# Kernel tuning notes

Measured on AMD Instinct MI355X. Metric: run time of the kernel, lower is better.

Reference implementation:

```python
import jax, jax.numpy as jnp
import numpy as np

# Output order of the stacked loss vector (7,):
# [loss_pose_intra_t, loss_pose_inter_t, loss_pose_intra_s, loss_pose_inter_s,
#  loss_pose_t, loss_pose_s, loss_pose]
ALPHA_T = 0.5
ALPHA_S = 0.75
ALPHA_TS = 0.5
EPS = 1e-8


def setup_inputs() -> dict:
    key = jax.random.key(0)
    k1, k2 = jax.random.split(key)
    B, M, C = 32, 784, 4
    pred_dT = jax.random.normal(k1, (B, M, M, C), dtype=jnp.float32)
    gt_dT = jax.random.normal(k2, (B, M, M, C), dtype=jnp.float32)
    # V=4 views, 196 tokens each; sum(Ms) must equal M
    Ms = jnp.full((4,), 196, dtype=jnp.int32)
    return {"pred_dT": pred_dT, "gt_dT": gt_dT, "Ms": Ms}


def reference(pred_dT, gt_dT, Ms):
    B, M, _, C = pred_dT.shape
    V = Ms.shape[0]
    dtype = pred_dT.dtype

    # criterion = 'mse', reduction='none'
    loss_full = (pred_dT - gt_dT) ** 2  # (B, M, M, C)

    # view id per token; same-view (intra) pair mask (M, M)
    view_ids = jnp.repeat(jnp.arange(V), Ms, total_repeat_length=M)
    intra_mask = (view_ids[:, None] == view_ids[None, :]).astype(dtype)

    # per-channel sums over all pairs and over intra-view pairs
    per_ch_all = loss_full.sum(axis=(0, 1, 2))                       # (C,)
    per_ch_intra = jnp.einsum('bijc,ij->c', loss_full, intra_mask)   # (C,)

    total_all_t = per_ch_all[0:2].sum()
    total_all_s = per_ch_all[2:4].sum()
    total_intra_t = per_ch_intra[0:2].sum()
    total_intra_s = per_ch_intra[2:4].sum()
    total_inter_t = total_all_t - total_intra_t
    total_inter_s = total_all_s - total_intra_s

    sum_Ms_sq = jnp.sum(Ms * Ms)
    diag_count = (sum_Ms_sq * B).astype(dtype)
    offdiag_count = ((M * M - sum_Ms_sq) * B).astype(dtype)

    zero = jnp.zeros((), dtype)
    loss_intra_t = jnp.where(diag_count > EPS, total_intra_t / diag_count, zero)
    loss_inter_t = jnp.where(offdiag_count > EPS, total_inter_t / offdiag_count, zero)
    loss_intra_s = jnp.where(diag_count > EPS, total_intra_s / diag_count, zero)
    loss_inter_s = jnp.where(offdiag_count > EPS, total_inter_s / offdiag_count, zero)

    loss_t = ALPHA_T * loss_inter_t + (1.0 - ALPHA_T) * loss_intra_t
    loss_s = ALPHA_S * loss_inter_s + (1.0 - ALPHA_S) * loss_intra_s
    loss = ALPHA_TS * loss_t + (1.0 - ALPHA_TS) * loss_s

    return jnp.stack([loss_intra_t, loss_inter_t, loss_intra_s, loss_inter_s,
                      loss_t, loss_s, loss])
```

## Files before the change

### kernel.cpp

```cpp
#include <hip/hip_runtime.h>

constexpr int B_ = 32;
constexpr int M_ = 784;

constexpr int NBLK = 1792;
constexpr int NTHR = 256;
constexpr int TOTAL  = B_ * M_ * M_;
constexpr int STRIDE = NBLK * NTHR;
constexpr int KFULL  = TOTAL / STRIDE;

constexpr float ALPHA_T  = 0.5f;
constexpr float ALPHA_S  = 0.75f;
constexpr float ALPHA_TS = 0.5f;
constexpr float EPS      = 1e-8f;

__global__ __launch_bounds__(NTHR) void pose_loss_partial_kernel(
    const float4* __restrict__ pred, const float4* __restrict__ gt,
    const int* __restrict__ Ms, float4* __restrict__ partials)
{
    const int cum0 = Ms[0];
    const int cum1 = cum0 + Ms[1];
    const int cum2 = cum1 + Ms[2];

    float all_t = 0.f, all_s = 0.f, intra_t = 0.f, intra_s = 0.f;

    auto body = [&](int idx) {
        const float4 p = pred[idx];
        const float4 g = gt[idx];
        const float d0 = p.x - g.x;
        const float d1 = p.y - g.y;
        const float d2 = p.z - g.z;
        const float d3 = p.w - g.w;
        const float t = d0 * d0 + d1 * d1;
        const float s = d2 * d2 + d3 * d3;
        all_t += t;
        all_s += s;
        const int q = idx / M_;
        const int j = idx - q * M_;
        const int i = q - (q / M_) * M_;
        const int vi = (i >= cum0) + (i >= cum1) + (i >= cum2);
        const int vj = (j >= cum0) + (j >= cum1) + (j >= cum2);
        if (vi == vj) { intra_t += t; intra_s += s; }
    };

    int idx = blockIdx.x * NTHR + threadIdx.x;
    #pragma unroll 2
    for (int k = 0; k < KFULL; ++k, idx += STRIDE) {
        body(idx);
    }
    if (idx < TOTAL) {
        body(idx);
    }

    float v0 = all_t, v1 = all_s, v2 = intra_t, v3 = intra_s;
    #pragma unroll
    for (int off = 32; off > 0; off >>= 1) {
        v0 += __shfl_down(v0, off, 64);
        v1 += __shfl_down(v1, off, 64);
        v2 += __shfl_down(v2, off, 64);
        v3 += __shfl_down(v3, off, 64);
    }

    __shared__ float4 sm[NTHR / 64];
    const int lane = threadIdx.x & 63;
    const int wid  = threadIdx.x >> 6;
    if (lane == 0) sm[wid] = make_float4(v0, v1, v2, v3);
    __syncthreads();

    if (threadIdx.x == 0) {
        float4 acc = sm[0];
        #pragma unroll
        for (int w = 1; w < NTHR / 64; ++w) {
            acc.x += sm[w].x; acc.y += sm[w].y;
            acc.z += sm[w].z; acc.w += sm[w].w;
        }
        partials[blockIdx.x] = acc;
    }
}

__global__ __launch_bounds__(NTHR) void pose_loss_final_kernel(
    const float4* __restrict__ partials, const int* __restrict__ Ms,
    float* __restrict__ out)
{
    float v0 = 0.f, v1 = 0.f, v2 = 0.f, v3 = 0.f;
    for (int p = threadIdx.x; p < NBLK; p += NTHR) {
        const float4 q = partials[p];
        v0 += q.x; v1 += q.y; v2 += q.z; v3 += q.w;
    }
    #pragma unroll
    for (int off = 32; off > 0; off >>= 1) {
        v0 += __shfl_down(v0, off, 64);
        v1 += __shfl_down(v1, off, 64);
        v2 += __shfl_down(v2, off, 64);
        v3 += __shfl_down(v3, off, 64);
    }
    __shared__ float4 sm[NTHR / 64];
    const int lane = threadIdx.x & 63;
    const int wid  = threadIdx.x >> 6;
    if (lane == 0) sm[wid] = make_float4(v0, v1, v2, v3);
    __syncthreads();

    if (threadIdx.x == 0) {
        float4 acc = sm[0];
        #pragma unroll
        for (int w = 1; w < NTHR / 64; ++w) {
            acc.x += sm[w].x; acc.y += sm[w].y;
            acc.z += sm[w].z; acc.w += sm[w].w;
        }
        const float total_all_t   = acc.x;
        const float total_all_s   = acc.y;
        const float total_intra_t = acc.z;
        const float total_intra_s = acc.w;
        const float total_inter_t = total_all_t - total_intra_t;
        const float total_inter_s = total_all_s - total_intra_s;

        int sum_Ms_sq = 0;
        #pragma unroll
        for (int v = 0; v < 4; ++v) sum_Ms_sq += Ms[v] * Ms[v];
        const float diag_count    = (float)((long long)sum_Ms_sq * B_);
        const float offdiag_count = (float)(((long long)M_ * M_ - sum_Ms_sq) * B_);

        const float li_t = (diag_count    > EPS) ? total_intra_t / diag_count    : 0.f;
        const float le_t = (offdiag_count > EPS) ? total_inter_t / offdiag_count : 0.f;
        const float li_s = (diag_count    > EPS) ? total_intra_s / diag_count    : 0.f;
        const float le_s = (offdiag_count > EPS) ? total_inter_s / offdiag_count : 0.f;

        const float loss_t = ALPHA_T  * le_t + (1.f - ALPHA_T)  * li_t;
        const float loss_s = ALPHA_S  * le_s + (1.f - ALPHA_S)  * li_s;
        const float loss   = ALPHA_TS * loss_t + (1.f - ALPHA_TS) * loss_s;

        out[0] = li_t;
        out[1] = le_t;
        out[2] = li_s;
        out[3] = le_s;
        out[4] = loss_t;
        out[5] = loss_s;
        out[6] = loss;
    }
}

extern "C" void kernel_launch(void* const* d_in, const int* in_sizes, int n_in,
                              void* d_out, int out_size, void* d_ws, size_t ws_size,
                              hipStream_t stream) {
    const float4* pred = (const float4*)d_in[0];
    const float4* gt   = (const float4*)d_in[1];
    const int*    Ms   = (const int*)d_in[2];
    float*        out  = (float*)d_out;
    float4*       partials = (float4*)d_ws;

    pose_loss_partial_kernel<<<NBLK, NTHR, 0, stream>>>(pred, gt, Ms, partials);
    pose_loss_final_kernel<<<1, NTHR, 0, stream>>>(partials, Ms, out);
}
```

Measured before the change: 113.0 us.

## Fuse partial and final reduction via last-block atomic counter; use contiguous per-block chunks

Replaces the two-kernel reduction with one kernel in which each block writes its partial sums, bumps an atomic counter, and the last block to finish does the final reduction and loss math. It also changes the work split from a grid-strided loop to contiguous per-block chunks on a 2048-block grid, with a launch-bounds occupancy hint. A memset of the counter is added before launch, and the old two-kernel path is kept as a fallback when the workspace is too small. The aim is to remove the second kernel launch and its dependency gap, at the cost of an extra memset launch and atomic traffic.

```diff
diff --git a/kernel.cpp b/kernel.cpp
--- a/kernel.cpp
+++ b/kernel.cpp
@@ -3,20 +3,54 @@
 constexpr int B_ = 32;
 constexpr int M_ = 784;
 
-constexpr int NBLK = 1792;
+constexpr int NBLK = 2048;
 constexpr int NTHR = 256;
-constexpr int TOTAL  = B_ * M_ * M_;
-constexpr int STRIDE = NBLK * NTHR;
-constexpr int KFULL  = TOTAL / STRIDE;
+constexpr int TOTAL = B_ * M_ * M_;
+constexpr int PER_BLOCK = TOTAL / NBLK;
+constexpr int KFULL = PER_BLOCK / NTHR;
+constexpr int TAILN = PER_BLOCK - KFULL * NTHR;
 
 constexpr float ALPHA_T  = 0.5f;
 constexpr float ALPHA_S  = 0.75f;
 constexpr float ALPHA_TS = 0.5f;
 constexpr float EPS      = 1e-8f;
 
-__global__ __launch_bounds__(NTHR) void pose_loss_partial_kernel(
+__device__ __forceinline__ void final_math(float total_all_t, float total_all_s,
+                                           float total_intra_t, float total_intra_s,
+                                           const int* __restrict__ Ms,
+                                           float* __restrict__ out)
+{
+    const float total_inter_t = total_all_t - total_intra_t;
+    const float total_inter_s = total_all_s - total_intra_s;
+
+    int sum_Ms_sq = 0;
+    #pragma unroll
+    for (int v = 0; v < 4; ++v) sum_Ms_sq += Ms[v] * Ms[v];
+    const float diag_count    = (float)((long long)sum_Ms_sq * B_);
+    const float offdiag_count = (float)(((long long)M_ * M_ - sum_Ms_sq) * B_);
+
+    const float li_t = (diag_count    > EPS) ? total_intra_t / diag_count    : 0.f;
+    const float le_t = (offdiag_count > EPS) ? total_inter_t / offdiag_count : 0.f;
+    const float li_s = (diag_count    > EPS) ? total_intra_s / diag_count    : 0.f;
+    const float le_s = (offdiag_count > EPS) ? total_inter_s / offdiag_count : 0.f;
+
+    const float loss_t = ALPHA_T  * le_t + (1.f - ALPHA_T)  * li_t;
+    const float loss_s = ALPHA_S  * le_s + (1.f - ALPHA_S)  * li_s;
+    const float loss   = ALPHA_TS * loss_t + (1.f - ALPHA_TS) * loss_s;
+
+    out[0] = li_t;
+    out[1] = le_t;
+    out[2] = li_s;
+    out[3] = le_s;
+    out[4] = loss_t;
+    out[5] = loss_s;
+    out[6] = loss;
+}
+
+__global__ __launch_bounds__(NTHR, 8) void pose_loss_fused_kernel(
     const float4* __restrict__ pred, const float4* __restrict__ gt,
-    const int* __restrict__ Ms, float4* __restrict__ partials)
+    const int* __restrict__ Ms, float* __restrict__ out,
+    int* __restrict__ counter, float* __restrict__ partials )
 {
     const int cum0 = Ms[0];
     const int cum1 = cum0 + Ms[1];
@@ -43,14 +77,10 @@
         if (vi == vj) { intra_t += t; intra_s += s; }
     };
 
-    int idx = blockIdx.x * NTHR + threadIdx.x;
+    int idx = blockIdx.x * PER_BLOCK + threadIdx.x;
     #pragma unroll 2
-    for (int k = 0; k < KFULL; ++k, idx += STRIDE) {
-        body(idx);
-    }
-    if (idx < TOTAL) {
-        body(idx);
-    }
+    for (int k = 0; k < KFULL; ++k, idx += NTHR) body(idx);
+    if (threadIdx.x < TAILN) body(idx);
 
     float v0 = all_t, v1 = all_s, v2 = intra_t, v3 = intra_s;
     #pragma unroll
@@ -62,6 +92,7 @@
     }
 
     __shared__ float4 sm[NTHR / 64];
+    __shared__ int slast;
     const int lane = threadIdx.x & 63;
     const int wid  = threadIdx.x >> 6;
     if (lane == 0) sm[wid] = make_float4(v0, v1, v2, v3);
@@ -74,19 +105,76 @@
             acc.x += sm[w].x; acc.y += sm[w].y;
             acc.z += sm[w].z; acc.w += sm[w].w;
         }
-        partials[blockIdx.x] = acc;
-    }
-}
-
-__global__ __launch_bounds__(NTHR) void pose_loss_final_kernel(
-    const float4* __restrict__ partials, const int* __restrict__ Ms,
-    float* __restrict__ out)
-{
-    float v0 = 0.f, v1 = 0.f, v2 = 0.f, v3 = 0.f;
+        float* pp = partials + (size_t)blockIdx.x * 4;
+        __hip_atomic_store(pp + 0, acc.x, __ATOMIC_RELAXED, __HIP_MEMORY_SCOPE_AGENT);
+        __hip_atomic_store(pp + 1, acc.y, __ATOMIC_RELAXED, __HIP_MEMORY_SCOPE_AGENT);
+        __hip_atomic_store(pp + 2, acc.z, __ATOMIC_RELAXED, __HIP_MEMORY_SCOPE_AGENT);
+        __hip_atomic_store(pp + 3, acc.w, __ATOMIC_RELAXED, __HIP_MEMORY_SCOPE_AGENT);
+        const int prev = __hip_atomic_fetch_add(counter, 1, __ATOMIC_ACQ_REL,
+                                                __HIP_MEMORY_SCOPE_AGENT);
+        slast = (prev == NBLK - 1) ? 1 : 0;
+    }
+    __syncthreads();
+    if (slast == 0) return;
+
+    float r0 = 0.f, r1 = 0.f, r2 = 0.f, r3 = 0.f;
     for (int p = threadIdx.x; p < NBLK; p += NTHR) {
-        const float4 q = partials[p];
-        v0 += q.x; v1 += q.y; v2 += q.z; v3 += q.w;
-    }
+        const float* pp = partials + (size_t)p * 4;
+        r0 += __hip_atomic_load(pp + 0, __ATOMIC_RELAXED, __HIP_MEMORY_SCOPE_AGENT);
+        r1 += __hip_atomic_load(pp + 1, __ATOMIC_RELAXED, __HIP_MEMORY_SCOPE_AGENT);
+        r2 += __hip_atomic_load(pp + 2, __ATOMIC_RELAXED, __HIP_MEMORY_SCOPE_AGENT);
+        r3 += __hip_atomic_load(pp + 3, __ATOMIC_RELAXED, __HIP_MEMORY_SCOPE_AGENT);
+    }
+    #pragma unroll
+    for (int off = 32; off > 0; off >>= 1) {
+        r0 += __shfl_down(r0, off, 64);
+        r1 += __shfl_down(r1, off, 64);
+        r2 += __shfl_down(r2, off, 64);
+        r3 += __shfl_down(r3, off, 64);
+    }
+    if (lane == 0) sm[wid] = make_float4(r0, r1, r2, r3);
+    __syncthreads();
+
+    if (threadIdx.x == 0) {
+        float4 acc = sm[0];
+        #pragma unroll
+        for (int w = 1; w < NTHR / 64; ++w) {
+            acc.x += sm[w].x; acc.y += sm[w].y;
+            acc.z += sm[w].z; acc.w += sm[w].w;
+        }
+        final_math(acc.x, acc.y, acc.z, acc.w, Ms, out);
+    }
+}
+
+__global__ __launch_bounds__(NTHR) void pose_loss_partial_kernel(
+    const float4* __restrict__ pred, const float4* __restrict__ gt,
+    const int* __restrict__ Ms, float4* __restrict__ partials)
+{
+    const int cum0 = Ms[0];
+    const int cum1 = cum0 + Ms[1];
+    const int cum2 = cum1 + Ms[2];
+
+    float all_t = 0.f, all_s = 0.f, intra_t = 0.f, intra_s = 0.f;
+    for (int idx = blockIdx.x * NTHR + threadIdx.x; idx < TOTAL;
+         idx += gridDim.x * NTHR) {
+        const float4 p = pred[idx];
+        const float4 g = gt[idx];
+        const float d0 = p.x - g.x;
+        const float d1 = p.y - g.y;
+        const float d2 = p.z - g.z;
+        const float d3 = p.w - g.w;
+        const float t = d0 * d0 + d1 * d1;
+        const float s = d2 * d2 + d3 * d3;
+        all_t += t; all_s += s;
+        const int q = idx / M_;
+        const int j = idx - q * M_;
+        const int i = q - (q / M_) * M_;
+        const int vi = (i >= cum0) + (i >= cum1) + (i >= cum2);
+        const int vj = (j >= cum0) + (j >= cum1) + (j >= cum2);
+        if (vi == vj) { intra_t += t; intra_s += s; }
+    }
+
+    float v0 = all_t, v1 = all_s, v2 = intra_t, v3 = intra_s;
     #pragma unroll
     for (int off = 32; off > 0; off >>= 1) {
         v0 += __shfl_down(v0, off, 64);
@@ -99,43 +187,46 @@
     const int wid  = threadIdx.x >> 6;
     if (lane == 0) sm[wid] = make_float4(v0, v1, v2, v3);
     __syncthreads();
-
-    if (threadIdx.x == 0) {
-        float4 acc = sm[0];
-        #pragma unroll
-        for (int w = 1; w < NTHR / 64; ++w) {
-            acc.x += sm[w].x; acc.y += sm[w].y;
-            acc.z += sm[w].z; acc.w += sm[w].w;
-        }
-        const float total_all_t   = acc.x;
-        const float total_all_s   = acc.y;
-        const float total_intra_t = acc.z;
-        const float total_intra_s = acc.w;
-        const float total_inter_t = total_all_t - total_intra_t;
-        const float total_inter_s = total_all_s - total_intra_s;
-
-        int sum_Ms_sq = 0;
-        #pragma unroll
-        for (int v = 0; v < 4; ++v) sum_Ms_sq += Ms[v] * Ms[v];
-        const float diag_count    = (float)((long long)sum_Ms_sq * B_);
-        const float offdiag_count = (float)(((long long)M_ * M_ - sum_Ms_sq) * B_);
-
-        const float li_t = (diag_count    > EPS) ? total_intra_t / diag_count    : 0.f;
-        const float le_t = (offdiag_count > EPS) ? total_inter_t / offdiag_count : 0.f;
-        const float li_s = (diag_count    > EPS) ? total_intra_s / diag_count    : 0.f;
-        const float le_s = (offdiag_count > EPS) ? total_inter_s / offdiag_count : 0.f;
-
-        const float loss_t = ALPHA_T  * le_t + (1.f - ALPHA_T)  * li_t;
-        const float loss_s = ALPHA_S  * le_s + (1.f - ALPHA_S)  * li_s;
-        const float loss   = ALPHA_TS * loss_t + (1.f - ALPHA_TS) * loss_s;
-
-        out[0] = li_t;
-        out[1] = le_t;
-        out[2] = li_s;
-        out[3] = le_s;
-        out[4] = loss_t;
-        out[5] = loss_s;
-        out[6] = loss;
+    if (threadIdx.x == 0) {
+        float4 acc = sm[0];
+        #pragma unroll
+        for (int w = 1; w < NTHR / 64; ++w) {
+            acc.x += sm[w].x; acc.y += sm[w].y;
+            acc.z += sm[w].z; acc.w += sm[w].w;
+        }
+        partials[blockIdx.x] = acc;
+    }
+}
+
+__global__ __launch_bounds__(NTHR) void pose_loss_final_kernel(
+    const float4* __restrict__ partials, int nprt, const int* __restrict__ Ms,
+    float* __restrict__ out)
+{
+    float v0 = 0.f, v1 = 0.f, v2 = 0.f, v3 = 0.f;
+    for (int p = threadIdx.x; p < nprt; p += NTHR) {
+        const float4 q = partials[p];
+        v0 += q.x; v1 += q.y; v2 += q.z; v3 += q.w;
+    }
+    #pragma unroll
+    for (int off = 32; off > 0; off >>= 1) {
+        v0 += __shfl_down(v0, off, 64);
+        v1 += __shfl_down(v1, off, 64);
+        v2 += __shfl_down(v2, off, 64);
+        v3 += __shfl_down(v3, off, 64);
+    }
+    __shared__ float4 sm[NTHR / 64];
+    const int lane = threadIdx.x & 63;
+    const int wid  = threadIdx.x >> 6;
+    if (lane == 0) sm[wid] = make_float4(v0, v1, v2, v3);
+    __syncthreads();
+    if (threadIdx.x == 0) {
+        float4 acc = sm[0];
+        #pragma unroll
+        for (int w = 1; w < NTHR / 64; ++w) {
+            acc.x += sm[w].x; acc.y += sm[w].y;
+            acc.z += sm[w].z; acc.w += sm[w].w;
+        }
+        final_math(acc.x, acc.y, acc.z, acc.w, Ms, out);
     }
 }
 
@@ -146,8 +237,18 @@
     const float4* gt   = (const float4*)d_in[1];
     const int*    Ms   = (const int*)d_in[2];
     float*        out  = (float*)d_out;
-    float4*       partials = (float4*)d_ws;
-
-    pose_loss_partial_kernel<<<NBLK, NTHR, 0, stream>>>(pred, gt, Ms, partials);
-    pose_loss_final_kernel<<<1, NTHR, 0, stream>>>(partials, Ms, out);
-}
+
+    const size_t fused_need = 16 + (size_t)NBLK * 16;
+    if (ws_size >= fused_need) {
+        int*   counter  = (int*)d_ws;
+        float* partials = (float*)((char*)d_ws + 16);
+        hipMemsetAsync(d_ws, 0, 16, stream);
+        pose_loss_fused_kernel<<<NBLK, NTHR, 0, stream>>>(pred, gt, Ms, out,
+                                                          counter, partials);
+    } else {
+        const int nblk = 1792;
+        float4* partials = (float4*)d_ws;
+        pose_loss_partial_kernel<<<nblk, NTHR, 0, stream>>>(pred, gt, Ms, partials);
+        pose_loss_final_kernel<<<1, NTHR, 0, stream>>>(partials, nblk, Ms, out);
+    }
+}
```

Measured after the change: 217.5 us. 1.93x slower.
